# Performance work log

Measured on AMD Instinct MI355X. Metric: run time of the kernel, lower is better.

Reference implementation:

```python
import jax, jax.numpy as jnp
import numpy as np

HIDDEN = 4096
RANK = 4
DELTA = 1.0
BATCH = 4096


def glorot(key, shape):
    return jax.random.uniform(key, shape, minval=-1.0, maxval=1.0) * jnp.sqrt(2.0 / sum(shape))


def setup_inputs() -> dict:
    key = jax.random.key(0)
    k1, k2, k3, k4, k5, k6 = jax.random.split(key, 6)
    return {
        "h": jax.random.normal(k5, (BATCH, HIDDEN), dtype=jnp.float32),
        "x": jax.random.normal(k6, (BATCH, HIDDEN), dtype=jnp.float32),
        "a_diag": glorot(k1, (HIDDEN,)),
        "p_vec": glorot(k2, (HIDDEN, RANK)),
        "q_vec": glorot(k3, (HIDDEN, RANK)),
        "b_mat": glorot(k4, (HIDDEN, HIDDEN)),
    }


def reference(h, x, a_diag, p_vec, q_vec, b_mat):
    # Per-sample original math: (I + delta*(diag(a) + p q^T)) @ h + delta * b_mat.T @ x
    # Batched (rows of h/x are samples) with the Woodbury-style low-rank form:
    #   A_disc @ h  ->  h + delta*(a*h + (h @ q) @ p^T)
    #   B_disc^T @ x -> delta * (x @ b_mat)
    Ah = h + DELTA * (h * a_diag + (h @ q_vec) @ p_vec.T)  # [B, N]
    Bx = DELTA * (x @ b_mat)                               # [B, N]
    return Ah + Bx
```

## Files before the change

### kernel.cpp

```cpp
#include <hip/hip_runtime.h>
#include <hip/hip_bf16.h>
#include <stdint.h>
#include <stddef.h>

#define HIDDEN 4096
#define BATCH  4096
#define RANK   4

typedef _Float16 f16;
typedef __attribute__((ext_vector_type(8))) _Float16 half8;
typedef __attribute__((ext_vector_type(4))) float f32x4;
typedef __attribute__((ext_vector_type(8))) unsigned short ushort8;

#define ASYNC_COPY16(g, l)                                                     \
  __builtin_amdgcn_global_load_lds(                                            \
      (__attribute__((address_space(1))) void*)(g),                            \
      (__attribute__((address_space(3))) void*)(l), 16, 0, 0)

__global__ void cast_f16_kernel(const float* __restrict__ src, f16* __restrict__ dst) {
  size_t i = ((size_t)blockIdx.x * blockDim.x + threadIdx.x) * 8;
  float4 v0 = *(const float4*)(src + i);
  float4 v1 = *(const float4*)(src + i + 4);
  union { f16 h[8]; ushort8 v; } u;
  u.h[0] = (f16)v0.x; u.h[1] = (f16)v0.y; u.h[2] = (f16)v0.z; u.h[3] = (f16)v0.w;
  u.h[4] = (f16)v1.x; u.h[5] = (f16)v1.y; u.h[6] = (f16)v1.z; u.h[7] = (f16)v1.w;
  *(ushort8*)(dst + i) = u.v;
}

__global__ void transpose_cast_kernel(const float* __restrict__ B, f16* __restrict__ Bt) {
  __shared__ __align__(16) f16 tile[64 * 64];
  const int t = threadIdx.x;
  const int bx = blockIdx.x;
  const int by = blockIdx.y;
  const int tx = t & 15, ty = t >> 4;
  #pragma unroll
  for (int i = 0; i < 4; i++) {
    const int k = ty + i * 16;
    float4 v = *(const float4*)(B + (size_t)(by * 64 + k) * HIDDEN + bx * 64 + tx * 4);
    f16 hv[4];
    hv[0] = (f16)v.x; hv[1] = (f16)v.y; hv[2] = (f16)v.z; hv[3] = (f16)v.w;
    #pragma unroll
    for (int c = 0; c < 4; c++) {
      const int n = tx * 4 + c;
      const int phys = (k >> 3) ^ ((n >> 2) & 7);
      tile[n * 64 + phys * 8 + (k & 7)] = hv[c];
    }
  }
  __syncthreads();
  const int wx = t & 7, wy = t >> 3;
  #pragma unroll
  for (int i = 0; i < 2; i++) {
    const int n = wy + i * 32;
    const int phys = wx ^ ((n >> 2) & 7);
    ushort8 v = *(ushort8*)&tile[n * 64 + phys * 8];
    *(ushort8*)(Bt + (size_t)(bx * 64 + n) * HIDDEN + by * 64 + wx * 8) = v;
  }
}

__global__ void hq_kernel(const float* __restrict__ h, const float* __restrict__ q,
                          float* __restrict__ hq) {
  const int b = blockIdx.x;
  const float* hrow = h + (size_t)b * HIDDEN;
  float a0 = 0.f, a1 = 0.f, a2 = 0.f, a3 = 0.f;
  for (int k = threadIdx.x; k < HIDDEN; k += 256) {
    float hv = hrow[k];
    float4 qv = *(const float4*)(q + (size_t)k * RANK);
    a0 += hv * qv.x; a1 += hv * qv.y; a2 += hv * qv.z; a3 += hv * qv.w;
  }
  #pragma unroll
  for (int off = 32; off; off >>= 1) {
    a0 += __shfl_down(a0, off, 64);
    a1 += __shfl_down(a1, off, 64);
    a2 += __shfl_down(a2, off, 64);
    a3 += __shfl_down(a3, off, 64);
  }
  __shared__ float red[4][4];
  const int wave = threadIdx.x >> 6, lane = threadIdx.x & 63;
  if (lane == 0) { red[wave][0] = a0; red[wave][1] = a1; red[wave][2] = a2; red[wave][3] = a3; }
  __syncthreads();
  if (threadIdx.x < 4) {
    float s = red[0][threadIdx.x] + red[1][threadIdx.x] + red[2][threadIdx.x] + red[3][threadIdx.x];
    hq[(size_t)b * RANK + threadIdx.x] = s;
  }
}

#define GBM 256
#define GBN 256
#define GBK 64

#define BARRIER()                                   \
  do {                                              \
    asm volatile("" ::: "memory");                  \
    __builtin_amdgcn_s_barrier();                   \
    asm volatile("" ::: "memory");                  \
  } while (0)

#define VMWAIT0() asm volatile("s_waitcnt vmcnt(0)" ::: "memory")
#define SBAR() __builtin_amdgcn_sched_barrier(0)

#define STAGE_ALL(SBUF)                                                      \
  do {                                                                       \
    char* ad_ = (char*)(&As[SBUF][0]) + wave * 1024;                         \
    char* bd_ = (char*)(&Bs[SBUF][0]) + wave * 1024;                         \
    ASYNC_COPY16(bg + (size_t)0 * 64 * HIDDEN, bd_ + 0 * 8192);              \
    ASYNC_COPY16(bg + (size_t)1 * 64 * HIDDEN, bd_ + 1 * 8192);              \
    ASYNC_COPY16(bg + (size_t)2 * 64 * HIDDEN, bd_ + 2 * 8192);              \
    ASYNC_COPY16(bg + (size_t)3 * 64 * HIDDEN, bd_ + 3 * 8192);              \
    ASYNC_COPY16(ag + (size_t)0 * 64 * HIDDEN, ad_ + 0 * 8192);              \
    ASYNC_COPY16(ag + (size_t)1 * 64 * HIDDEN, ad_ + 1 * 8192);              \
    ASYNC_COPY16(ag + (size_t)2 * 64 * HIDDEN, ad_ + 2 * 8192);              \
    ASYNC_COPY16(ag + (size_t)3 * 64 * HIDDEN, ad_ + 3 * 8192);              \
    ag += GBK; bg += GBK;                                                    \
  } while (0)

#define LDF(base, R16, SG) (*(const half8*)((base) + (R16) * (16 * GBK) + (SG)))

#define MQUAD(I0, AF, BF)                                                               \
  __builtin_amdgcn_s_setprio(1);                                                        \
  acc[I0+0][0] = __builtin_amdgcn_mfma_f32_16x16x32_f16(AF[0], BF[0], acc[I0+0][0], 0, 0, 0); \
  acc[I0+0][1] = __builtin_amdgcn_mfma_f32_16x16x32_f16(AF[0], BF[1], acc[I0+0][1], 0, 0, 0); \
  acc[I0+0][2] = __builtin_amdgcn_mfma_f32_16x16x32_f16(AF[0], BF[2], acc[I0+0][2], 0, 0, 0); \
  acc[I0+0][3] = __builtin_amdgcn_mfma_f32_16x16x32_f16(AF[0], BF[3], acc[I0+0][3], 0, 0, 0); \
  acc[I0+1][0] = __builtin_amdgcn_mfma_f32_16x16x32_f16(AF[1], BF[0], acc[I0+1][0], 0, 0, 0); \
  acc[I0+1][1] = __builtin_amdgcn_mfma_f32_16x16x32_f16(AF[1], BF[1], acc[I0+1][1], 0, 0, 0); \
  acc[I0+1][2] = __builtin_amdgcn_mfma_f32_16x16x32_f16(AF[1], BF[2], acc[I0+1][2], 0, 0, 0); \
  acc[I0+1][3] = __builtin_amdgcn_mfma_f32_16x16x32_f16(AF[1], BF[3], acc[I0+1][3], 0, 0, 0); \
  acc[I0+2][0] = __builtin_amdgcn_mfma_f32_16x16x32_f16(AF[2], BF[0], acc[I0+2][0], 0, 0, 0); \
  acc[I0+2][1] = __builtin_amdgcn_mfma_f32_16x16x32_f16(AF[2], BF[1], acc[I0+2][1], 0, 0, 0); \
  acc[I0+2][2] = __builtin_amdgcn_mfma_f32_16x16x32_f16(AF[2], BF[2], acc[I0+2][2], 0, 0, 0); \
  acc[I0+2][3] = __builtin_amdgcn_mfma_f32_16x16x32_f16(AF[2], BF[3], acc[I0+2][3], 0, 0, 0); \
  acc[I0+3][0] = __builtin_amdgcn_mfma_f32_16x16x32_f16(AF[3], BF[0], acc[I0+3][0], 0, 0, 0); \
  acc[I0+3][1] = __builtin_amdgcn_mfma_f32_16x16x32_f16(AF[3], BF[1], acc[I0+3][1], 0, 0, 0); \
  acc[I0+3][2] = __builtin_amdgcn_mfma_f32_16x16x32_f16(AF[3], BF[2], acc[I0+3][2], 0, 0, 0); \
  acc[I0+3][3] = __builtin_amdgcn_mfma_f32_16x16x32_f16(AF[3], BF[3], acc[I0+3][3], 0, 0, 0); \
  __builtin_amdgcn_s_setprio(0);

#define TILE(BUF, SBUF, DO_STAGE)                                            \
  {                                                                          \
    const f16* Ab_ = &As[BUF][0] + (wm * 128 + fm) * GBK;                    \
    const f16* Bb_ = &Bs[BUF][0] + (wn * 64 + fm) * GBK;                     \
    const int sg0_ = (q ^ sw) * 8;                                           \
    const int sg1_ = ((4 + q) ^ sw) * 8;                                     \
    half8 aA[4], aB[4], bE[4], bO[4];                                        \
    BARRIER();                                                               \
                                                    \
    aA[0] = LDF(Ab_, 0, sg0_); aA[1] = LDF(Ab_, 1, sg0_);                    \
    aA[2] = LDF(Ab_, 2, sg0_); aA[3] = LDF(Ab_, 3, sg0_);                    \
    bE[0] = LDF(Bb_, 0, sg0_); bE[1] = LDF(Bb_, 1, sg0_);                    \
    bE[2] = LDF(Bb_, 2, sg0_); bE[3] = LDF(Bb_, 3, sg0_);                    \
    if (DO_STAGE) STAGE_ALL(SBUF);                                           \
                                                  \
    aB[0] = LDF(Ab_, 4, sg0_); aB[1] = LDF(Ab_, 5, sg0_);                    \
    aB[2] = LDF(Ab_, 6, sg0_); aB[3] = LDF(Ab_, 7, sg0_);                    \
    SBAR();                                                                  \
    MQUAD(0, aA, bE)               \
                        \
    aA[0] = LDF(Ab_, 0, sg1_); aA[1] = LDF(Ab_, 1, sg1_);                    \
    aA[2] = LDF(Ab_, 2, sg1_); aA[3] = LDF(Ab_, 3, sg1_);                    \
    bO[0] = LDF(Bb_, 0, sg1_); bO[1] = LDF(Bb_, 1, sg1_);                    \
    bO[2] = LDF(Bb_, 2, sg1_); bO[3] = LDF(Bb_, 3, sg1_);                    \
    SBAR();                                                                  \
    MQUAD(4, aB, bE)                                         \
                                                  \
    aB[0] = LDF(Ab_, 4, sg1_); aB[1] = LDF(Ab_, 5, sg1_);                    \
    aB[2] = LDF(Ab_, 6, sg1_); aB[3] = LDF(Ab_, 7, sg1_);                    \
    SBAR();                                                                  \
    MQUAD(0, aA, bO)                                         \
    MQUAD(4, aB, bO)                                         \
    if (DO_STAGE) { VMWAIT0(); }                                             \
  }

__global__ __launch_bounds__(512, 2) void gemm_fused_kernel(
    const f16* __restrict__ Xb, const f16* __restrict__ Bt,
    const float* __restrict__ h, const float* __restrict__ a_diag,
    const float* __restrict__ p_vec, const float* __restrict__ hq,
    float* __restrict__ out) {
  __shared__ __align__(16) f16 As[2][GBM * GBK];
  __shared__ __align__(16) f16 Bs[2][GBN * GBK];
  const int tid = threadIdx.x;
  const int lin = blockIdx.x + (blockIdx.y << 4);
  const int xk = lin & 7, xr = lin >> 3;
  const int bm = ((xk & 3) << 2) | (xr & 3);
  const int bn = ((xk >> 2) << 3) | (xr >> 2);
  const int wave = tid >> 6, lane = tid & 63;
  const int wm = wave >> 2, wn = wave & 3;

  const int srow = tid >> 3;
  const int gseg = (tid & 7) ^ (srow & 7);
  const f16* ag = Xb + (size_t)(bm * GBM + srow) * HIDDEN + gseg * 8;
  const f16* bg = Bt + (size_t)(bn * GBN + srow) * HIDDEN + gseg * 8;

  f32x4 acc[8][4];
  #pragma unroll
  for (int i = 0; i < 8; i++)
    #pragma unroll
    for (int j = 0; j < 4; j++)
      acc[i][j] = (f32x4){0.f, 0.f, 0.f, 0.f};

  const int q = lane >> 4;
  const int fm = lane & 15;
  const int sw = fm & 7;

  STAGE_ALL(0);
  VMWAIT0();

  #pragma unroll 1
  for (int kt2 = 0; kt2 < 31; ++kt2) {
    TILE(0, 1, 1)
    TILE(1, 0, 1)
  }
  TILE(0, 1, 1)
  TILE(1, 0, 0)

  float ad[4];
  float4 pv[4];
  #pragma unroll
  for (int j = 0; j < 4; j++) {
    const int gn = bn * GBN + wn * 64 + j * 16 + fm;
    ad[j] = 1.0f + a_diag[gn];
    pv[j] = *(const float4*)(p_vec + (size_t)gn * RANK);
  }
  #pragma unroll
  for (int i = 0; i < 8; i++) {
    #pragma unroll
    for (int r = 0; r < 4; r++) {
      const size_t gb = (size_t)(bm * GBM + wm * 128 + i * 16 + q * 4 + r);
      const float4 hv = *(const float4*)(hq + gb * RANK);
      const size_t rowoff = gb * HIDDEN + bn * GBN + wn * 64 + fm;
      #pragma unroll
      for (int j = 0; j < 4; j++) {
        const size_t idx = rowoff + j * 16;
        const float hval = __builtin_nontemporal_load(&h[idx]);
        const float v = acc[i][j][r] + hval * ad[j] +
                        hv.x * pv[j].x + hv.y * pv[j].y + hv.z * pv[j].z + hv.w * pv[j].w;
        __builtin_nontemporal_store(v, &out[idx]);
      }
    }
  }
}

__global__ void gemm_f32_fallback_kernel(const float* __restrict__ x, const float* __restrict__ bmat,
                                         const float* __restrict__ h, const float* __restrict__ a_diag,
                                         const float* __restrict__ p_vec, const float* __restrict__ hq,
                                         float* __restrict__ out) {
  __shared__ float As[16][64];
  __shared__ float Bs[16][68];
  const int t = threadIdx.x;
  const int bx = blockIdx.x, by = blockIdx.y;
  const int tm = t & 15, tn = t >> 4;
  float acc[4][4] = {{0.f}};
  for (int k0 = 0; k0 < HIDDEN; k0 += 16) {
    #pragma unroll
    for (int l = 0; l < 4; l++) {
      int idx = t + l * 256;
      int r = idx >> 4, k = idx & 15;
      As[k][r] = x[(size_t)(by * 64 + r) * HIDDEN + k0 + k];
      int kb = idx >> 6, nb = idx & 63;
      Bs[kb][nb] = bmat[(size_t)(k0 + kb) * HIDDEN + bx * 64 + nb];
    }
    __syncthreads();
    #pragma unroll
    for (int k = 0; k < 16; k++) {
      float av[4], bv[4];
      #pragma unroll
      for (int ii = 0; ii < 4; ii++) av[ii] = As[k][tm * 4 + ii];
      #pragma unroll
      for (int jj = 0; jj < 4; jj++) bv[jj] = Bs[k][tn * 4 + jj];
      #pragma unroll
      for (int ii = 0; ii < 4; ii++)
        #pragma unroll
        for (int jj = 0; jj < 4; jj++)
          acc[ii][jj] += av[ii] * bv[jj];
    }
    __syncthreads();
  }
  #pragma unroll
  for (int jj = 0; jj < 4; jj++) {
    int gn = bx * 64 + tn * 4 + jj;
    float ad = 1.0f + a_diag[gn];
    float4 pv = *(const float4*)(p_vec + (size_t)gn * RANK);
    #pragma unroll
    for (int ii = 0; ii < 4; ii++) {
      size_t gb = (size_t)(by * 64 + tm * 4 + ii);
      float4 hv = *(const float4*)(hq + gb * RANK);
      size_t idx = gb * HIDDEN + gn;
      out[idx] = acc[ii][jj] + h[idx] * ad +
                 hv.x * pv.x + hv.y * pv.y + hv.z * pv.z + hv.w * pv.w;
    }
  }
}

extern "C" void kernel_launch(void* const* d_in, const int* in_sizes, int n_in,
                              void* d_out, int out_size, void* d_ws, size_t ws_size,
                              hipStream_t stream) {
  const float* h      = (const float*)d_in[0];
  const float* x      = (const float*)d_in[1];
  const float* a_diag = (const float*)d_in[2];
  const float* p_vec  = (const float*)d_in[3];
  const float* q_vec  = (const float*)d_in[4];
  const float* b_mat  = (const float*)d_in[5];
  float* out = (float*)d_out;

  const size_t nElem = (size_t)BATCH * HIDDEN;
  const size_t hq_bytes = (size_t)BATCH * RANK * sizeof(float);
  const size_t need = hq_bytes + 2 * nElem * sizeof(f16);

  float* hq = (float*)d_ws;
  hq_kernel<<<BATCH, 256, 0, stream>>>(h, q_vec, hq);

  if (ws_size >= need) {
    f16* Xb = (f16*)((char*)d_ws + hq_bytes);
    f16* Bt = Xb + nElem;
    cast_f16_kernel<<<nElem / 2048, 256, 0, stream>>>(x, Xb);
    transpose_cast_kernel<<<dim3(HIDDEN / 64, HIDDEN / 64), 256, 0, stream>>>(b_mat, Bt);
    gemm_fused_kernel<<<dim3(BATCH / GBM, HIDDEN / GBN), 512, 0, stream>>>(
        Xb, Bt, h, a_diag, p_vec, hq, out);
  } else {
    gemm_f32_fallback_kernel<<<dim3(HIDDEN / 64, BATCH / 64), 256, 0, stream>>>(
        x, b_mat, h, a_diag, p_vec, hq, out);
  }
}
```

Before: 358.4 us.

## Split GEMM K-tile into half-K sub-buffers with finer-grained async staging

Reorganizes LDS into four 256x32 sub-buffers per stage (A/B for each K-half) and issues the async global->LDS copies in four chunks interleaved with the MFMA phases. Partial vmcnt waits (vmcnt(4)) let compute on the first half proceed while the second half is still arriving, and the swizzle is changed to fit 32-wide rows. It adds many more barriers and explicit lgkmcnt waits per tile, which could serialize LDS reads with MFMAs. That extra synchronization may cancel out the overlap gain.

Measured after the change: 356.4 us. No clear change (-0.6%).

```diff
diff --git a/kernel.cpp b/kernel.cpp
--- a/kernel.cpp
+++ b/kernel.cpp
@@ -95,28 +95,29 @@
     asm volatile("" ::: "memory");                  \
   } while (0)
 
+#define LGKM0()                                                 \
+  do {                                                          \
+    asm volatile("s_waitcnt lgkmcnt(0)" ::: "memory");          \
+    __builtin_amdgcn_sched_barrier(0);                          \
+  } while (0)
+
 #define VMWAIT0() asm volatile("s_waitcnt vmcnt(0)" ::: "memory")
-#define SBAR() __builtin_amdgcn_sched_barrier(0)
-
-#define STAGE_ALL(SBUF)                                                      \
+#define VMWAIT4() asm volatile("s_waitcnt vmcnt(4)" ::: "memory")
+#define VMNOP()   do { } while (0)
+
+#define RB128 ((size_t)128 * HIDDEN)
+
+#define STAGE_U(S, U, PTR, KH)                                               \
   do {                                                                       \
-    char* ad_ = (char*)(&As[SBUF][0]) + wave * 1024;                         \
-    char* bd_ = (char*)(&Bs[SBUF][0]) + wave * 1024;                         \
-    ASYNC_COPY16(bg + (size_t)0 * 64 * HIDDEN, bd_ + 0 * 8192);              \
-    ASYNC_COPY16(bg + (size_t)1 * 64 * HIDDEN, bd_ + 1 * 8192);              \
-    ASYNC_COPY16(bg + (size_t)2 * 64 * HIDDEN, bd_ + 2 * 8192);              \
-    ASYNC_COPY16(bg + (size_t)3 * 64 * HIDDEN, bd_ + 3 * 8192);              \
-    ASYNC_COPY16(ag + (size_t)0 * 64 * HIDDEN, ad_ + 0 * 8192);              \
-    ASYNC_COPY16(ag + (size_t)1 * 64 * HIDDEN, ad_ + 1 * 8192);              \
-    ASYNC_COPY16(ag + (size_t)2 * 64 * HIDDEN, ad_ + 2 * 8192);              \
-    ASYNC_COPY16(ag + (size_t)3 * 64 * HIDDEN, ad_ + 3 * 8192);              \
-    ag += GBK; bg += GBK;                                                    \
+    char* d_ = (char*)(&L[S][U][0]) + wave * 1024;                           \
+    ASYNC_COPY16(PTR + (KH) * 32, d_);                                       \
+    ASYNC_COPY16(PTR + (KH) * 32 + RB128, d_ + 8192);                        \
   } while (0)
 
-#define LDF(base, R16, SG) (*(const half8*)((base) + (R16) * (16 * GBK) + (SG)))
-
-#define MQUAD(I0, AF, BF)                                                               \
-  __builtin_amdgcn_s_setprio(1);                                                        \
+#define RD(base, i) (*(const half8*)((base) + (i) * 512))
+
+#define MFMA16(I0, AF, BF)                                                                    \
+  __builtin_amdgcn_s_setprio(1);                                                              \
   acc[I0+0][0] = __builtin_amdgcn_mfma_f32_16x16x32_f16(AF[0], BF[0], acc[I0+0][0], 0, 0, 0); \
   acc[I0+0][1] = __builtin_amdgcn_mfma_f32_16x16x32_f16(AF[0], BF[1], acc[I0+0][1], 0, 0, 0); \
   acc[I0+0][2] = __builtin_amdgcn_mfma_f32_16x16x32_f16(AF[0], BF[2], acc[I0+0][2], 0, 0, 0); \
@@ -135,39 +136,51 @@
   acc[I0+3][3] = __builtin_amdgcn_mfma_f32_16x16x32_f16(AF[3], BF[3], acc[I0+3][3], 0, 0, 0); \
   __builtin_amdgcn_s_setprio(0);
 
-#define TILE(BUF, SBUF, DO_STAGE)                                            \
+#define TILE8(BUF, SBUF, DO_STAGE, W1, W3)                                   \
   {                                                                          \
-    const f16* Ab_ = &As[BUF][0] + (wm * 128 + fm) * GBK;                    \
-    const f16* Bb_ = &Bs[BUF][0] + (wn * 64 + fm) * GBK;                     \
-    const int sg0_ = (q ^ sw) * 8;                                           \
-    const int sg1_ = ((4 + q) ^ sw) * 8;                                     \
-    half8 aA[4], aB[4], bE[4], bO[4];                                        \
-    BARRIER();                                                               \
-                                                    \
-    aA[0] = LDF(Ab_, 0, sg0_); aA[1] = LDF(Ab_, 1, sg0_);                    \
-    aA[2] = LDF(Ab_, 2, sg0_); aA[3] = LDF(Ab_, 3, sg0_);                    \
-    bE[0] = LDF(Bb_, 0, sg0_); bE[1] = LDF(Bb_, 1, sg0_);                    \
-    bE[2] = LDF(Bb_, 2, sg0_); bE[3] = LDF(Bb_, 3, sg0_);                    \
-    if (DO_STAGE) STAGE_ALL(SBUF);                                           \
-                                                  \
-    aB[0] = LDF(Ab_, 4, sg0_); aB[1] = LDF(Ab_, 5, sg0_);                    \
-    aB[2] = LDF(Ab_, 6, sg0_); aB[3] = LDF(Ab_, 7, sg0_);                    \
-    SBAR();                                                                  \
-    MQUAD(0, aA, bE)               \
-                        \
-    aA[0] = LDF(Ab_, 0, sg1_); aA[1] = LDF(Ab_, 1, sg1_);                    \
-    aA[2] = LDF(Ab_, 2, sg1_); aA[3] = LDF(Ab_, 3, sg1_);                    \
-    bO[0] = LDF(Bb_, 0, sg1_); bO[1] = LDF(Bb_, 1, sg1_);                    \
-    bO[2] = LDF(Bb_, 2, sg1_); bO[3] = LDF(Bb_, 3, sg1_);                    \
-    SBAR();                                                                  \
-    MQUAD(4, aB, bE)                                         \
-                                                  \
-    aB[0] = LDF(Ab_, 4, sg1_); aB[1] = LDF(Ab_, 5, sg1_);                    \
-    aB[2] = LDF(Ab_, 6, sg1_); aB[3] = LDF(Ab_, 7, sg1_);                    \
-    SBAR();                                                                  \
-    MQUAD(0, aA, bO)                                         \
-    MQUAD(4, aB, bO)                                         \
-    if (DO_STAGE) { VMWAIT0(); }                                             \
+    const f16* A0_ = &L[BUF][0][0] + (wm * 128 + fm) * 32 + pseg * 8;        \
+    const f16* B0_ = &L[BUF][1][0] + (wn * 64 + fm) * 32 + pseg * 8;         \
+    const f16* A1_ = &L[BUF][2][0] + (wm * 128 + fm) * 32 + pseg * 8;        \
+    const f16* B1_ = &L[BUF][3][0] + (wn * 64 + fm) * 32 + pseg * 8;         \
+    half8 aA[4], bB[4];                                                      \
+                                           \
+    aA[0] = RD(A0_, 0); aA[1] = RD(A0_, 1);                                  \
+    aA[2] = RD(A0_, 2); aA[3] = RD(A0_, 3);                                  \
+    bB[0] = RD(B0_, 0); bB[1] = RD(B0_, 1);                                  \
+    bB[2] = RD(B0_, 2); bB[3] = RD(B0_, 3);                                  \
+    if (DO_STAGE) STAGE_U(SBUF, 0, ag, 0);                                   \
+    BARRIER();                                                               \
+    LGKM0();                                                                 \
+    MFMA16(0, aA, bB)                                                        \
+    BARRIER();                                                               \
+                                          \
+    aA[0] = RD(A0_, 4); aA[1] = RD(A0_, 5);                                  \
+    aA[2] = RD(A0_, 6); aA[3] = RD(A0_, 7);                                  \
+    if (DO_STAGE) STAGE_U(SBUF, 1, bg, 0);                                   \
+    BARRIER();                                                               \
+    LGKM0();                                                                 \
+    MFMA16(4, aA, bB)                                                        \
+    W1;                                                                      \
+    BARRIER();                                                               \
+                                           \
+    aA[0] = RD(A1_, 0); aA[1] = RD(A1_, 1);                                  \
+    aA[2] = RD(A1_, 2); aA[3] = RD(A1_, 3);                                  \
+    bB[0] = RD(B1_, 0); bB[1] = RD(B1_, 1);                                  \
+    bB[2] = RD(B1_, 2); bB[3] = RD(B1_, 3);                                  \
+    if (DO_STAGE) STAGE_U(SBUF, 2, ag, 1);                                   \
+    BARRIER();                                                               \
+    LGKM0();                                                                 \
+    MFMA16(0, aA, bB)                                                        \
+    BARRIER();                                                               \
+                                                      \
+    aA[0] = RD(A1_, 4); aA[1] = RD(A1_, 5);                                  \
+    aA[2] = RD(A1_, 6); aA[3] = RD(A1_, 7);                                  \
+    if (DO_STAGE) { STAGE_U(SBUF, 3, bg, 1); ag += GBK; bg += GBK; }         \
+    BARRIER();                                                               \
+    LGKM0();                                                                 \
+    MFMA16(4, aA, bB)                                                        \
+    W3;                                                                      \
+    BARRIER();                                                               \
   }
 
 __global__ __launch_bounds__(512, 2) void gemm_fused_kernel(
@@ -175,8 +188,7 @@
     const float* __restrict__ h, const float* __restrict__ a_diag,
     const float* __restrict__ p_vec, const float* __restrict__ hq,
     float* __restrict__ out) {
-  __shared__ __align__(16) f16 As[2][GBM * GBK];
-  __shared__ __align__(16) f16 Bs[2][GBN * GBK];
+  __shared__ __align__(16) f16 L[2][4][256 * 32];
   const int tid = threadIdx.x;
   const int lin = blockIdx.x + (blockIdx.y << 4);
   const int xk = lin & 7, xr = lin >> 3;
@@ -185,8 +197,8 @@
   const int wave = tid >> 6, lane = tid & 63;
   const int wm = wave >> 2, wn = wave & 3;
 
-  const int srow = tid >> 3;
-  const int gseg = (tid & 7) ^ (srow & 7);
+  const int srow = tid >> 2;
+  const int gseg = (tid & 3) ^ ((tid >> 3) & 3);
   const f16* ag = Xb + (size_t)(bm * GBM + srow) * HIDDEN + gseg * 8;
   const f16* bg = Bt + (size_t)(bn * GBN + srow) * HIDDEN + gseg * 8;
 
@@ -199,18 +211,23 @@
 
   const int q = lane >> 4;
   const int fm = lane & 15;
-  const int sw = fm & 7;
-
-  STAGE_ALL(0);
-  VMWAIT0();
+  const int pseg = q ^ ((fm >> 1) & 3);
+
+  STAGE_U(0, 0, ag, 0);
+  STAGE_U(0, 1, bg, 0);
+  STAGE_U(0, 2, ag, 1);
+  STAGE_U(0, 3, bg, 1);
+  ag += GBK; bg += GBK;
+  VMWAIT4();
+  BARRIER();
 
   #pragma unroll 1
   for (int kt2 = 0; kt2 < 31; ++kt2) {
-    TILE(0, 1, 1)
-    TILE(1, 0, 1)
-  }
-  TILE(0, 1, 1)
-  TILE(1, 0, 0)
+    TILE8(0, 1, 1, VMWAIT4(), VMWAIT4())
+    TILE8(1, 0, 1, VMWAIT4(), VMWAIT4())
+  }
+  TILE8(0, 1, 1, VMWAIT4(), VMWAIT4())
+  TILE8(1, 0, 0, VMWAIT0(), VMNOP())
 
   float ad[4];
   float4 pv[4];
```
